# Optimization experiments

Hardware: AMD Instinct MI355X
Metric: run time of the kernel (lower is better)

## Reference

```python
import jax, jax.numpy as jnp
import numpy as np

B, S, D = 4, 2048, 1024
LN_EPS = 1e-3  # Keras LayerNormalization default epsilon

def setup_inputs() -> dict:
    key = jax.random.key(0)
    ks = jax.random.split(key, 7)
    s = D ** -0.5
    return {
        "x": jax.random.normal(ks[0], (B, S, D), dtype=jnp.float32),
        "Wq": jax.random.normal(ks[1], (D, D), dtype=jnp.float32) * s,
        "bq": jnp.zeros((D,), dtype=jnp.float32),
        "Wk": jax.random.normal(ks[2], (D, D), dtype=jnp.float32) * s,
        "bk": jnp.zeros((D,), dtype=jnp.float32),
        "Wv": jax.random.normal(ks[3], (D, D), dtype=jnp.float32) * s,
        "bv": jnp.zeros((D,), dtype=jnp.float32),
        "gamma": jnp.ones((D,), dtype=jnp.float32),
        "beta": jnp.zeros((D,), dtype=jnp.float32),
    }

def reference(x, Wq, bq, Wk, bk, Wv, bv, gamma, beta):
    q = jnp.einsum('bsd,de->bse', x, Wq) + bq
    k = jnp.einsum('bsd,de->bse', x, Wk) + bk
    v = jnp.einsum('bsd,de->bse', x, Wv) + bv
    scale = jnp.asarray(k.shape[-1], x.dtype) ** -0.5
    scores = jnp.einsum('bqd,bkd->bqk', q, k) * scale  # [B,S,S]
    weights = jax.nn.softmax(scores, axis=-1)
    attn = jnp.einsum('bqk,bkd->bqd', weights, v)
    h = x + attn
    mu = jnp.mean(h, axis=-1, keepdims=True)
    var = jnp.mean(jnp.square(h - mu), axis=-1, keepdims=True)
    return gamma * (h - mu) * jax.lax.rsqrt(var + LN_EPS) + beta
```

## Files before the change

kernel.cpp:

```cpp
#include <hip/hip_runtime.h>

typedef __attribute__((ext_vector_type(8))) short bf16x8;
typedef __attribute__((ext_vector_type(4))) float f32x4;

__device__ __forceinline__ unsigned short f2bf(float f) {
    union { float f; unsigned int u; } v; v.f = f;
    unsigned int u = v.u;
    u += 0x7fffu + ((u >> 16) & 1u);
    return (unsigned short)(u >> 16);
}
__device__ __forceinline__ float bf2f(unsigned short s) {
    union { unsigned int u; float f; } v; v.u = ((unsigned int)s) << 16;
    return v.f;
}

__device__ __forceinline__ void gload16(const unsigned short* g, unsigned short* l) {
    __builtin_amdgcn_global_load_lds(
        (const __attribute__((address_space(1))) unsigned int*)(unsigned long long)(g),
        (__attribute__((address_space(3))) unsigned int*)(unsigned int)(unsigned long long)(l),
        16, 0, 0);
}

#define MFMA16(a, b, c) __builtin_amdgcn_mfma_f32_16x16x32_bf16((a), (b), (c), 0, 0, 0)

__global__ __launch_bounds__(256) void detect_dtype(
    const unsigned short* __restrict__ x, int* __restrict__ flag) {
    __shared__ int red[4];
    const int t = threadIdx.x;
    int cnt = 0;
    #pragma unroll
    for (int i = 0; i < 16; i++) {
        const unsigned short v = x[t * 16 + i];
        const int e = (v >> 7) & 0xFF;
        cnt += (e >= 0xC8) ? 1 : 0;
    }
    #pragma unroll
    for (int off = 32; off; off >>= 1) cnt += __shfl_down(cnt, off);
    if ((t & 63) == 0) red[t >> 6] = cnt;
    __syncthreads();
    if (t == 0) *flag = (red[0] + red[1] + red[2] + red[3] >= 16) ? 1 : 0;
}

__global__ __launch_bounds__(256) void convert_x(
    const void* __restrict__ xin, unsigned short* __restrict__ xb,
    const int* __restrict__ flag) {
    const long i = ((long)blockIdx.x * 256 + threadIdx.x) * 4;
    if (*flag) {
        const float4 v = *(const float4*)((const float*)xin + i);
        unsigned long long pk =  (unsigned long long)f2bf(v.x)
                              | ((unsigned long long)f2bf(v.y) << 16)
                              | ((unsigned long long)f2bf(v.z) << 32)
                              | ((unsigned long long)f2bf(v.w) << 48);
        *(unsigned long long*)(xb + i) = pk;
    } else {
        *(unsigned long long*)(xb + i) =
            *(const unsigned long long*)((const unsigned short*)xin + i);
    }
}

__global__ __launch_bounds__(256) void transpose_convert(
    const void* __restrict__ W, unsigned short* __restrict__ Wt,
    const int* __restrict__ flag) {
    __shared__ unsigned short tile[32][33];
    const int tx = threadIdx.x & 31, ty = threadIdx.x >> 5;
    const int x0 = blockIdx.x * 32, y0 = blockIdx.y * 32;
    const int f = *flag;
    #pragma unroll
    for (int i = 0; i < 32; i += 8) {
        const long idx = (long)(y0 + ty + i) * 1024 + x0 + tx;
        tile[ty + i][tx] = f ? f2bf(((const float*)W)[idx])
                             : ((const unsigned short*)W)[idx];
    }
    __syncthreads();
    #pragma unroll
    for (int i = 0; i < 32; i += 8)
        Wt[(long)(x0 + ty + i) * 1024 + y0 + tx] = tile[tx][ty + i];
}

__global__ __launch_bounds__(256) void convert_vec1024(
    const void* __restrict__ in, unsigned short* __restrict__ outv,
    const int* __restrict__ flag) {
    const int i = threadIdx.x * 4;
    if (*flag) {
        const float4 v = *(const float4*)((const float*)in + i);
        outv[i] = f2bf(v.x); outv[i+1] = f2bf(v.y);
        outv[i+2] = f2bf(v.z); outv[i+3] = f2bf(v.w);
    } else {
        *(unsigned long long*)(outv + i) =
            *(const unsigned long long*)((const unsigned short*)in + i);
    }
}

__global__ __launch_bounds__(256, 3) void gemm128(
    const unsigned short* __restrict__ A, const unsigned short* __restrict__ Bt,
    unsigned short* __restrict__ C,
    int K, int lda, int ldb, int ldc,
    long strideAz, long strideBz, long strideCz,
    const unsigned short* __restrict__ bias, float scale) {

    const int gx = gridDim.x, gy = gridDim.y;
    const int nwg = gx * gy * (int)gridDim.z;
    int bid = (int)blockIdx.x + gx * ((int)blockIdx.y + gy * (int)blockIdx.z);
    {
        const int q = nwg >> 3, r = nwg & 7;
        const int xcd = bid & 7, idx = bid >> 3;
        bid = (xcd < r ? xcd * (q + 1) : r * (q + 1) + (xcd - r) * q) + idx;
    }
    const int bz  = bid / (gx * gy);
    const int rmd = bid - bz * gx * gy;
    const int by  = rmd / gx;
    const int bx  = rmd - by * gx;

    A  += (long)bz * strideAz;
    Bt += (long)bz * strideBz;
    C  += (long)bz * strideCz;

    __shared__ unsigned short lds[24576];

    const int tid  = threadIdx.x;
    const int wave = tid >> 6;
    const int lane = tid & 63;
    const int quad = lane >> 4;
    const int lm   = lane & 15;
    const int wm   = (wave >> 1) * 64;
    const int wn   = (wave & 1) * 64;

    const int m0 = by * 128;
    const int n0 = bx * 128;

    const int rloc = wave * 16 + ((lane >> 2) & 15);
    const int cch  = (((lane & 3) - ((lane >> 4) & 3)) & 3) ^ ((lane >> 2) & 3);
    const unsigned short* pA = A  + (long)(m0 + rloc) * lda + cch * 8;
    const unsigned short* pB = Bt + (long)(n0 + rloc) * ldb + cch * 8;
    const long sA = 64L * lda, sB = 64L * ldb;

    const int fs   = ((quad ^ (lm & 3)) + (lm >> 2)) & 3;
    const int aoff = (wm + lm) * 32 + fs * 8;
    const int boff = 4096 + (wn + lm) * 32 + fs * 8;

    f32x4 acc[4][4];
    #pragma unroll
    for (int i = 0; i < 4; i++)
        #pragma unroll
        for (int j = 0; j < 4; j++) acc[i][j] = (f32x4){0.f, 0.f, 0.f, 0.f};

    const int NT = K >> 5;

#define STAGE(kt) do {                                              \
        unsigned short* db_ = lds + ((kt) % 3) * 8192 + wave * 512; \
        const unsigned short* ga_ = pA + (long)(kt) * 32;           \
        const unsigned short* gb_ = pB + (long)(kt) * 32;           \
        gload16(ga_,      db_);                                     \
        gload16(ga_ + sA, db_ + 2048);                              \
        gload16(gb_,      db_ + 4096);                              \
        gload16(gb_ + sB, db_ + 6144);                              \
    } while (0)

    STAGE(0); STAGE(1);
    asm volatile("s_waitcnt vmcnt(4)" ::: "memory");
    __builtin_amdgcn_s_barrier();

    for (int kt = 0; kt < NT; ++kt) {
        const unsigned short* buf = lds + (kt % 3) * 8192;

        if (kt + 2 < NT) STAGE(kt + 2);
        bf16x8 aF[4], bF[4];
        #pragma unroll
        for (int i = 0; i < 4; i++) aF[i] = *(const bf16x8*)&buf[aoff + i * 512];
        #pragma unroll
        for (int j = 0; j < 4; j++) bF[j] = *(const bf16x8*)&buf[boff + j * 512];

        __builtin_amdgcn_s_setprio(1);
        #pragma unroll
        for (int i = 0; i < 4; i++)
            #pragma unroll
            for (int j = 0; j < 4; j++)
                acc[i][j] = MFMA16(aF[i], bF[j], acc[i][j]);
        __builtin_amdgcn_s_setprio(0);

        if (kt + 2 < NT) { asm volatile("s_waitcnt vmcnt(4)" ::: "memory"); }
        else             { asm volatile("s_waitcnt vmcnt(0)" ::: "memory"); }
        __builtin_amdgcn_s_barrier();
    }
#undef STAGE

    {
        unsigned short* ep = lds + wave * 4096;
        #pragma unroll
        for (int i = 0; i < 4; i++) {
            float b4[4] = {0.f, 0.f, 0.f, 0.f};
            if (bias) {
                const unsigned short* bp = bias + m0 + wm + i * 16 + quad * 4;
                #pragma unroll
                for (int r = 0; r < 4; r++) b4[r] = bf2f(bp[r]);
            }
            #pragma unroll
            for (int j = 0; j < 4; j++) {
                unsigned long long pk = 0;
                #pragma unroll
                for (int r = 0; r < 4; r++)
                    pk |= (unsigned long long)f2bf((acc[i][j][r] + b4[r]) * scale) << (16 * r);
                *(unsigned long long*)&ep[(j * 16 + lm) * 64 + (((i * 4 + quad) ^ lm) << 2)] = pk;
            }
        }
        const int m8 = lane & 15;
        #pragma unroll
        for (int it = 0; it < 16; it++) {
            const int n = it * 4 + (lane >> 4);
            const unsigned long long v =
                *(const unsigned long long*)&ep[n * 64 + ((m8 ^ (n & 15)) << 2)];
            *(unsigned long long*)&C[(long)(n0 + wn + n) * ldc + m0 + wm + m8 * 4] = v;
        }
    }
}

__global__ __launch_bounds__(256) void softmax_rows(unsigned short* __restrict__ S, int rowlen) {
    __shared__ float red[4];
    const long row = blockIdx.x;
    unsigned short* p = S + row * rowlen;
    const int t = threadIdx.x;
    const int wave = t >> 6, lane = t & 63;

    uint4 raw = *(uint4*)(p + t * 8);
    unsigned short* u = (unsigned short*)&raw;
    float v[8], mx = -3.0e38f;
    #pragma unroll
    for (int i = 0; i < 8; i++) { v[i] = bf2f(u[i]); mx = fmaxf(mx, v[i]); }
    #pragma unroll
    for (int off = 32; off; off >>= 1) mx = fmaxf(mx, __shfl_down(mx, off));
    if (lane == 0) red[wave] = mx;
    __syncthreads();
    mx = fmaxf(fmaxf(red[0], red[1]), fmaxf(red[2], red[3]));
    __syncthreads();

    float s = 0.f;
    #pragma unroll
    for (int i = 0; i < 8; i++) { v[i] = __expf(v[i] - mx); s += v[i]; }
    #pragma unroll
    for (int off = 32; off; off >>= 1) s += __shfl_down(s, off);
    if (lane == 0) red[wave] = s;
    __syncthreads();
    s = red[0] + red[1] + red[2] + red[3];
    const float inv = 1.f / s;
    #pragma unroll
    for (int i = 0; i < 8; i++) u[i] = f2bf(v[i] * inv);
    *(uint4*)(p + t * 8) = raw;
}

__global__ __launch_bounds__(256) void resid_ln(
    const void* __restrict__ x, const unsigned short* __restrict__ attn,
    const void* __restrict__ gamma, const void* __restrict__ beta,
    void* __restrict__ out, const int* __restrict__ flag) {
    __shared__ float red[8];
    const long row = blockIdx.x;
    const int t = threadIdx.x;
    const int wave = t >> 6, lane = t & 63;
    const long base = row * 1024 + t * 4;
    const int f = *flag;

    uint2 ar = *(const uint2*)(attn + base);
    const unsigned short* au = (const unsigned short*)&ar;
    float h[4], s = 0.f, s2 = 0.f;
    if (f) {
        const float4 xr = *(const float4*)((const float*)x + base);
        h[0] = xr.x + bf2f(au[0]); h[1] = xr.y + bf2f(au[1]);
        h[2] = xr.z + bf2f(au[2]); h[3] = xr.w + bf2f(au[3]);
    } else {
        const uint2 xr = *(const uint2*)((const unsigned short*)x + base);
        const unsigned short* xu = (const unsigned short*)&xr;
        #pragma unroll
        for (int i = 0; i < 4; i++) h[i] = bf2f(xu[i]) + bf2f(au[i]);
    }
    #pragma unroll
    for (int i = 0; i < 4; i++) { s += h[i]; s2 += h[i] * h[i]; }
    #pragma unroll
    for (int off = 32; off; off >>= 1) { s += __shfl_down(s, off); s2 += __shfl_down(s2, off); }
    if (lane == 0) { red[wave] = s; red[4 + wave] = s2; }
    __syncthreads();
    s  = red[0] + red[1] + red[2] + red[3];
    s2 = red[4] + red[5] + red[6] + red[7];
    const float mu = s * (1.f / 1024.f);
    const float var = s2 * (1.f / 1024.f) - mu * mu;
    const float rstd = rsqrtf(var + 1e-3f);

    float g[4], bb[4];
    if (f) {
        const float4 gr = *(const float4*)((const float*)gamma + t * 4);
        const float4 br = *(const float4*)((const float*)beta  + t * 4);
        g[0]=gr.x; g[1]=gr.y; g[2]=gr.z; g[3]=gr.w;
        bb[0]=br.x; bb[1]=br.y; bb[2]=br.z; bb[3]=br.w;
    } else {
        #pragma unroll
        for (int i = 0; i < 4; i++) {
            g[i]  = bf2f(((const unsigned short*)gamma)[t * 4 + i]);
            bb[i] = bf2f(((const unsigned short*)beta)[t * 4 + i]);
        }
    }

    if (f) {
        float4 o;
        o.x = g[0]*(h[0]-mu)*rstd + bb[0];
        o.y = g[1]*(h[1]-mu)*rstd + bb[1];
        o.z = g[2]*(h[2]-mu)*rstd + bb[2];
        o.w = g[3]*(h[3]-mu)*rstd + bb[3];
        *(float4*)((float*)out + base) = o;
    } else {
        unsigned long long pk = 0;
        #pragma unroll
        for (int i = 0; i < 4; i++)
            pk |= (unsigned long long)f2bf(g[i]*(h[i]-mu)*rstd + bb[i]) << (16 * i);
        *(unsigned long long*)((unsigned short*)out + base) = pk;
    }
}

extern "C" void kernel_launch(void* const* d_in, const int* in_sizes, int n_in,
                              void* d_out, int out_size, void* d_ws, size_t ws_size,
                              hipStream_t stream) {
    const void* x  = d_in[0];
    const void* Wq = d_in[1];
    const void* bq = d_in[2];
    const void* Wk = d_in[3];
    const void* bk = d_in[4];
    const void* Wv = d_in[5];
    const void* bv = d_in[6];
    const void* gamma = d_in[7];
    const void* beta  = d_in[8];

    char* ws = (char*)d_ws;
    unsigned short* xb   = (unsigned short*)(ws);
    unsigned short* attn = (unsigned short*)(ws);
    unsigned short* wt   = (unsigned short*)(ws + 16777216L);
    unsigned short* bb   = (unsigned short*)(ws + 23068672L);
    int*            flag = (int*)(ws + 23074816L);
    unsigned short* qk   = (unsigned short*)(ws + 23074944L);
    unsigned short* vt   = (unsigned short*)(ws + 56629376L);
    unsigned short* sc   = (unsigned short*)(ws + 73406592L);

    const dim3 tb(256);
    detect_dtype<<<dim3(1), tb, 0, stream>>>((const unsigned short*)x, flag);
    convert_x<<<dim3(8192), tb, 0, stream>>>(x, xb, flag);
    transpose_convert<<<dim3(32, 32), tb, 0, stream>>>(Wq, wt, flag);
    transpose_convert<<<dim3(32, 32), tb, 0, stream>>>(Wk, wt + 1048576, flag);
    transpose_convert<<<dim3(32, 32), tb, 0, stream>>>(Wv, wt + 2097152, flag);
    convert_vec1024<<<dim3(1), tb, 0, stream>>>(bq, bb, flag);
    convert_vec1024<<<dim3(1), tb, 0, stream>>>(bk, bb + 1024, flag);
    convert_vec1024<<<dim3(1), tb, 0, stream>>>(bv, bb + 2048, flag);

    gemm128<<<dim3(64, 16, 1), tb, 0, stream>>>(wt, xb, qk,
        1024, 1024, 1024, 2048, 0L, 0L, 0L, bb, 1.0f);
    gemm128<<<dim3(8, 64, 1), tb, 0, stream>>>(xb, wt + 2097152, vt,
        1024, 1024, 1024, 8192, 0L, 0L, 0L, nullptr, 1.0f);
    gemm128<<<dim3(16, 16, 4), tb, 0, stream>>>(qk + 1024, qk, sc,
        1024, 2048, 2048, 2048, 4194304L, 4194304L, 4194304L, nullptr, 0.03125f);
    softmax_rows<<<dim3(8192), tb, 0, stream>>>(sc, 2048);
    gemm128<<<dim3(16, 8, 4), tb, 0, stream>>>(vt, sc, attn,
        2048, 8192, 2048, 1024, 2048L, 4194304L, 2097152L, bb + 2048, 1.0f);
    resid_ln<<<dim3(8192), tb, 0, stream>>>(x, attn, gamma, beta, d_out, flag);
}
```

Measured before the change: 307.2 us.

## Widen GEMM tiles to 128x256 with 512 threads and 64-deep K steps

The bf16 GEMM kernel now runs 8 waves per block and computes a 128x256 output tile instead of 128x128. Each main-loop step consumes 64 K elements rather than 32, and the LDS swizzle is reworked to match. The B fragments are loaded in two halves so the second half's loads can overlap the first batch of MFMAs. The aim is better operand reuse per byte loaded and fewer loop iterations and barriers, at the cost of much more LDS (144 KB triple-buffered), which allows at most one such block per CU.

```diff
diff --git a/kernel.cpp b/kernel.cpp
--- a/kernel.cpp
+++ b/kernel.cpp
@@ -91,7 +91,7 @@
     }
 }
 
-__global__ __launch_bounds__(256, 3) void gemm128(
+__global__ __launch_bounds__(512, 2) void gemm_bt(
     const unsigned short* __restrict__ A, const unsigned short* __restrict__ Bt,
     unsigned short* __restrict__ C,
     int K, int lda, int ldb, int ldc,
@@ -115,28 +115,31 @@
     Bt += (long)bz * strideBz;
     C  += (long)bz * strideCz;
 
-    __shared__ unsigned short lds[24576];
+    __shared__ unsigned short lds[73728];
 
     const int tid  = threadIdx.x;
     const int wave = tid >> 6;
     const int lane = tid & 63;
     const int quad = lane >> 4;
     const int lm   = lane & 15;
-    const int wm   = (wave >> 1) * 64;
-    const int wn   = (wave & 1) * 64;
+    const int wm   = (wave >> 2) * 64;
+    const int wn   = (wave & 3) * 64;
 
     const int m0 = by * 128;
-    const int n0 = bx * 128;
-
-    const int rloc = wave * 16 + ((lane >> 2) & 15);
-    const int cch  = (((lane & 3) - ((lane >> 4) & 3)) & 3) ^ ((lane >> 2) & 3);
-    const unsigned short* pA = A  + (long)(m0 + rloc) * lda + cch * 8;
-    const unsigned short* pB = Bt + (long)(n0 + rloc) * ldb + cch * 8;
-    const long sA = 64L * lda, sB = 64L * ldb;
-
-    const int fs   = ((quad ^ (lm & 3)) + (lm >> 2)) & 3;
-    const int aoff = (wm + lm) * 32 + fs * 8;
-    const int boff = 4096 + (wn + lm) * 32 + fs * 8;
+    const int n0 = bx * 256;
+
+    const int rl   = wave * 8 + (lane >> 3);
+    const int ksrc = (((lane & 7) ^ ((lane >> 3) & 7)) << 3);
+    const unsigned short* pA0 = A  + (long)(m0 + rl) * lda + ksrc;
+    const unsigned short* pB0 = Bt + (long)(n0 + rl) * ldb + ksrc;
+    const long sA1 = 64L * lda, sB1 = 64L * ldb;
+    const int wofs = wave * 512;
+
+    const int sx8 = lm & 7;
+    const int kq0 = ((quad ^ sx8) << 3);
+    const int kq1 = (((4 + quad) ^ sx8) << 3);
+    const int aro = (wm + lm) << 6;
+    const int bro = (wn + lm) << 6;
 
     f32x4 acc[4][4];
     #pragma unroll
@@ -144,41 +147,67 @@
         #pragma unroll
         for (int j = 0; j < 4; j++) acc[i][j] = (f32x4){0.f, 0.f, 0.f, 0.f};
 
-    const int NT = K >> 5;
-
-#define STAGE(kt) do {                                              \
-        unsigned short* db_ = lds + ((kt) % 3) * 8192 + wave * 512; \
-        const unsigned short* ga_ = pA + (long)(kt) * 32;           \
-        const unsigned short* gb_ = pB + (long)(kt) * 32;           \
-        gload16(ga_,      db_);                                     \
-        gload16(ga_ + sA, db_ + 2048);                              \
-        gload16(gb_,      db_ + 4096);                              \
-        gload16(gb_ + sB, db_ + 6144);                              \
+    const int NT = K >> 6;
+
+#define STAGE(kt) do {                                                    \
+        unsigned short* ab_ = &lds[((kt) % 3) * 24576 + wofs];            \
+        unsigned short* bb_ = ab_ + 8192;                                 \
+        const unsigned short* ga_ = pA0 + (long)(kt) * 64;                \
+        const unsigned short* gb_ = pB0 + (long)(kt) * 64;                \
+        gload16(ga_,            ab_);                                     \
+        gload16(ga_ + sA1,      ab_ + 4096);                              \
+        gload16(gb_,            bb_);                                     \
+        gload16(gb_ + sB1,      bb_ + 4096);                              \
+        gload16(gb_ + 2 * sB1,  bb_ + 8192);                              \
+        gload16(gb_ + 3 * sB1,  bb_ + 12288);                             \
     } while (0)
 
     STAGE(0); STAGE(1);
-    asm volatile("s_waitcnt vmcnt(4)" ::: "memory");
+    asm volatile("s_waitcnt vmcnt(6)" ::: "memory");
     __builtin_amdgcn_s_barrier();
 
     for (int kt = 0; kt < NT; ++kt) {
-        const unsigned short* buf = lds + (kt % 3) * 8192;
+        const unsigned short* ab = &lds[(kt % 3) * 24576];
+        const unsigned short* bb = ab + 8192;
 
         if (kt + 2 < NT) STAGE(kt + 2);
-        bf16x8 aF[4], bF[4];
-        #pragma unroll
-        for (int i = 0; i < 4; i++) aF[i] = *(const bf16x8*)&buf[aoff + i * 512];
-        #pragma unroll
-        for (int j = 0; j < 4; j++) bF[j] = *(const bf16x8*)&buf[boff + j * 512];
-
+
+        bf16x8 aM[4][2], bN[2][2], bN2[2][2];
+        #pragma unroll
+        for (int i = 0; i < 4; i++) {
+            aM[i][0] = *(const bf16x8*)&ab[aro + (i << 10) + kq0];
+            aM[i][1] = *(const bf16x8*)&ab[aro + (i << 10) + kq1];
+        }
+        #pragma unroll
+        for (int j = 0; j < 2; j++) {
+            bN[j][0] = *(const bf16x8*)&bb[bro + (j << 10) + kq0];
+            bN[j][1] = *(const bf16x8*)&bb[bro + (j << 10) + kq1];
+        }
         __builtin_amdgcn_s_setprio(1);
         #pragma unroll
         for (int i = 0; i < 4; i++)
             #pragma unroll
-            for (int j = 0; j < 4; j++)
-                acc[i][j] = MFMA16(aF[i], bF[j], acc[i][j]);
+            for (int j = 0; j < 2; j++) {
+                acc[i][j] = MFMA16(aM[i][0], bN[j][0], acc[i][j]);
+                acc[i][j] = MFMA16(aM[i][1], bN[j][1], acc[i][j]);
+            }
         __builtin_amdgcn_s_setprio(0);
-
-        if (kt + 2 < NT) { asm volatile("s_waitcnt vmcnt(4)" ::: "memory"); }
+        #pragma unroll
+        for (int j = 0; j < 2; j++) {
+            bN2[j][0] = *(const bf16x8*)&bb[bro + ((j + 2) << 10) + kq0];
+            bN2[j][1] = *(const bf16x8*)&bb[bro + ((j + 2) << 10) + kq1];
+        }
+        __builtin_amdgcn_s_setprio(1);
+        #pragma unroll
+        for (int i = 0; i < 4; i++)
+            #pragma unroll
+            for (int j = 0; j < 2; j++) {
+                acc[i][j + 2] = MFMA16(aM[i][0], bN2[j][0], acc[i][j + 2]);
+                acc[i][j + 2] = MFMA16(aM[i][1], bN2[j][1], acc[i][j + 2]);
+            }
+        __builtin_amdgcn_s_setprio(0);
+
+        if (kt + 2 < NT) { asm volatile("s_waitcnt vmcnt(6)" ::: "memory"); }
         else             { asm volatile("s_waitcnt vmcnt(0)" ::: "memory"); }
         __builtin_amdgcn_s_barrier();
     }
@@ -194,22 +223,24 @@
                 #pragma unroll
                 for (int r = 0; r < 4; r++) b4[r] = bf2f(bp[r]);
             }
+            const int c = i * 4 + quad;
+            const int s = c ^ lm;
             #pragma unroll
             for (int j = 0; j < 4; j++) {
                 unsigned long long pk = 0;
                 #pragma unroll
                 for (int r = 0; r < 4; r++)
                     pk |= (unsigned long long)f2bf((acc[i][j][r] + b4[r]) * scale) << (16 * r);
-                *(unsigned long long*)&ep[(j * 16 + lm) * 64 + (((i * 4 + quad) ^ lm) << 2)] = pk;
+                *(unsigned long long*)&ep[(j * 16 + lm) * 64 + (s << 2)] = pk;
             }
         }
-        const int m8 = lane & 15;
+        const int cc = lane & 15;
         #pragma unroll
         for (int it = 0; it < 16; it++) {
             const int n = it * 4 + (lane >> 4);
             const unsigned long long v =
-                *(const unsigned long long*)&ep[n * 64 + ((m8 ^ (n & 15)) << 2)];
-            *(unsigned long long*)&C[(long)(n0 + wn + n) * ldc + m0 + wm + m8 * 4] = v;
+                *(const unsigned long long*)&ep[n * 64 + ((cc ^ (n & 15)) << 2)];
+            *(unsigned long long*)&C[(long)(n0 + wn + n) * ldc + m0 + wm + cc * 4] = v;
         }
     }
 }
@@ -337,6 +368,7 @@
     unsigned short* sc   = (unsigned short*)(ws + 73406592L);
 
     const dim3 tb(256);
+    const dim3 tg(512);
     detect_dtype<<<dim3(1), tb, 0, stream>>>((const unsigned short*)x, flag);
     convert_x<<<dim3(8192), tb, 0, stream>>>(x, xb, flag);
     transpose_convert<<<dim3(32, 32), tb, 0, stream>>>(Wq, wt, flag);
@@ -346,14 +378,14 @@
     convert_vec1024<<<dim3(1), tb, 0, stream>>>(bk, bb + 1024, flag);
     convert_vec1024<<<dim3(1), tb, 0, stream>>>(bv, bb + 2048, flag);
 
-    gemm128<<<dim3(64, 16, 1), tb, 0, stream>>>(wt, xb, qk,
+    gemm_bt<<<dim3(32, 16, 1), tg, 0, stream>>>(wt, xb, qk,
         1024, 1024, 1024, 2048, 0L, 0L, 0L, bb, 1.0f);
-    gemm128<<<dim3(8, 64, 1), tb, 0, stream>>>(xb, wt + 2097152, vt,
+    gemm_bt<<<dim3(4, 64, 1), tg, 0, stream>>>(xb, wt + 2097152, vt,
         1024, 1024, 1024, 8192, 0L, 0L, 0L, nullptr, 1.0f);
-    gemm128<<<dim3(16, 16, 4), tb, 0, stream>>>(qk + 1024, qk, sc,
+    gemm_bt<<<dim3(8, 16, 4), tg, 0, stream>>>(qk + 1024, qk, sc,
         1024, 2048, 2048, 2048, 4194304L, 4194304L, 4194304L, nullptr, 0.03125f);
     softmax_rows<<<dim3(8192), tb, 0, stream>>>(sc, 2048);
-    gemm128<<<dim3(16, 8, 4), tb, 0, stream>>>(vt, sc, attn,
+    gemm_bt<<<dim3(8, 8, 4), tg, 0, stream>>>(vt, sc, attn,
         2048, 8192, 2048, 1024, 2048L, 4194304L, 2097152L, bb + 2048, 1.0f);
     resid_ln<<<dim3(8192), tb, 0, stream>>>(x, attn, gamma, beta, d_out, flag);
 }
```

After: 292.2 us. -4.9%, faster.
